# Optimization experiments

Measured on AMD Instinct MI355X. Metric: run time of the kernel, lower is better.

The kernel has to match this reference:

```python
import jax, jax.numpy as jnp
import numpy as np

NUM_HEADS = 8
NEG_INF = float(-2**32 + 1)  # matches torch padding value -2**32+1


def positional_encoding(B, T, d):
    # matches module: pe[:, :, 0::2] = sin(pos*div), pe[:, :, 1::2] = cos(pos*div)
    pos = jnp.arange(T, dtype=jnp.float32)[:, None]                      # (T, 1)
    div = jnp.exp(jnp.arange(0, d, 2, dtype=jnp.float32) * (-np.log(10000.0) / d))  # (d/2,)
    ang = pos * div                                                       # (T, d/2)
    pe = jnp.zeros((T, d), jnp.float32)
    pe = pe.at[:, 0::2].set(jnp.sin(ang)).at[:, 1::2].set(jnp.cos(ang))
    return jnp.broadcast_to(pe[None], (B, T, d))


def setup_inputs() -> dict:
    key = jax.random.key(0)
    ks = jax.random.split(key, 8)
    B, T, d, dff = 4, 2048, 128, 512
    s = 1.0 / np.sqrt(d)
    return {
        "x": jax.random.normal(ks[0], (B, T, d), jnp.float32),
        "W_Q": jax.random.normal(ks[1], (d, d), jnp.float32) * s,
        "W_K": jax.random.normal(ks[2], (d, d), jnp.float32) * s,
        "W_V": jax.random.normal(ks[3], (d, d), jnp.float32) * s,
        "W1": jax.random.normal(ks[4], (d, dff), jnp.float32) * s,
        "b1": jnp.zeros((dff,), jnp.float32),
        "W2": jax.random.normal(ks[5], (dff, d), jnp.float32) * (1.0 / np.sqrt(dff)),
        "b2": jnp.zeros((d,), jnp.float32),
    }


def reference(x, W_Q, W_K, W_V, W1, b1, W2, b2):
    B, T, d = x.shape
    H = NUM_HEADS
    e = d // H
    x = x + positional_encoding(B, T, d)           # residual later uses post-PE input
    Q = x @ W_Q
    K = x @ W_K
    V = x @ W_V
    # torch split(dim=2)+cat(dim=0) == (b t (h e)) -> (h b) t e; keep head axis separate
    Qh = Q.reshape(B, T, H, e).transpose(2, 0, 1, 3)   # (H, B, T, e)
    Kh = K.reshape(B, T, H, e).transpose(2, 0, 1, 3)
    Vh = V.reshape(B, T, H, e).transpose(2, 0, 1, 3)
    scores = jnp.einsum('hbqe,hbke->hbqk', Qh, Kh) / (T ** 0.5)  # scale by sqrt(time_step)
    mask = jnp.tril(jnp.ones((T, T), jnp.float32))
    scores = jnp.where(mask == 0, jnp.float32(NEG_INF), scores)
    # torch F.softmax(dim=1) on (H*B, T, T) -> softmax over QUERY axis (axis=2 here)
    attn = jax.nn.softmax(scores, axis=2)
    out = jnp.einsum('hbqk,hbke->hbqe', attn, Vh)      # (H, B, T, e)
    out = out.transpose(1, 2, 0, 3).reshape(B, T, d)   # cat heads back on feature dim
    ff = jnp.maximum(out @ W1 + b1, 0.0) @ W2 + b2
    return ff + x
```

## Files before the change

kernel.cpp:

```cpp
#include <hip/hip_runtime.h>
#include <math.h>
#include <stdint.h>

#define T_SEQ 2048
#define BATCH 4
#define DMODEL 128
#define DFF 512
#define NHEAD 8
#define EHEAD 16

#define QSCALE (0.022097086912079608f * 1.4426950408889634f)

typedef __attribute__((ext_vector_type(8))) short bf16x8;
typedef __attribute__((ext_vector_type(4))) short bf16x4;
typedef __attribute__((ext_vector_type(4))) float f32x4;

__device__ __forceinline__ short f2bf(float f) {
    uint32_t u = __float_as_uint(f);
    u = u + 0x7FFF + ((u >> 16) & 1);
    return (short)(u >> 16);
}
__device__ __forceinline__ short bftrunc(float f) {
    return (short)(__float_as_uint(f) >> 16);
}
__device__ __forceinline__ float bf2f(short s) {
    return __uint_as_float(((uint32_t)(unsigned short)s) << 16);
}
__device__ __forceinline__ float exp2_fast(float x) {
#if __has_builtin(__builtin_amdgcn_exp2f)
    return __builtin_amdgcn_exp2f(x);
#else
    float r; asm("v_exp_f32 %0, %1" : "=v"(r) : "v"(x)); return r;
#endif
}

#define MFMA16(A, B, C) __builtin_amdgcn_mfma_f32_16x16x32_bf16(A, B, C, 0, 0, 0)

__device__ __forceinline__ void gload16(const void* g, void* l) {
    __builtin_amdgcn_global_load_lds(
        (const __attribute__((address_space(1))) void*)g,
        (__attribute__((address_space(3))) void*)l, 16, 0, 0);
}

__device__ __forceinline__ int pair_rank(int id) {
    return (id < 256) ? id : 767 - id;
}

#define WP 136
__global__ __launch_bounds__(256) void k_qkv(const float* __restrict__ x,
                                             const float* __restrict__ WQ,
                                             const float* __restrict__ WK,
                                             const float* __restrict__ WV,
                                             const float* __restrict__ W1,
                                             const float* __restrict__ W2,
                                             float* __restrict__ xpe,
                                             short* __restrict__ Qh,
                                             short* __restrict__ Kh,
                                             short* __restrict__ Vs,
                                             short* __restrict__ W1t,
                                             short* __restrict__ W2t) {
    __shared__ __align__(16) short Wlds[128 * WP];
    int z = blockIdx.y;
    int tid = threadIdx.x;

    if (z == 3) {
        int base = (int)blockIdx.x * 256 + tid;
#pragma unroll
        for (int i = 0; i < 2; ++i) {
            int o = base + i * 32768;
            int n = o >> 7, k = o & 127;
            W1t[o] = f2bf(W1[k * 512 + n]);
        }
#pragma unroll
        for (int i = 0; i < 2; ++i) {
            int o = base + i * 32768;
            int n = o >> 9, k = o & 511;
            W2t[o] = f2bf(W2[k * 128 + n]);
        }
        return;
    }

    int wave = tid >> 6, lane = tid & 63;
    int g = lane >> 4, c = lane & 15;
    int row0 = blockIdx.x * 64 + wave * 16;
    int row = row0 + c;
    int tloc = row & (T_SEQ - 1);

    {
        const float* Wsrc = (z == 0) ? WQ : (z == 1) ? WK : WV;
        int k = tid & 127, n0 = (tid >> 7) * 64;
        const float* src = Wsrc + k * 128 + n0;
#pragma unroll
        for (int j = 0; j < 64; j += 4) {
            float4 wv = *(const float4*)(src + j);
            Wlds[(n0 + j + 0) * WP + k] = f2bf(wv.x);
            Wlds[(n0 + j + 1) * WP + k] = f2bf(wv.y);
            Wlds[(n0 + j + 2) * WP + k] = f2bf(wv.z);
            Wlds[(n0 + j + 3) * WP + k] = f2bf(wv.w);
        }
    }

    bf16x8 af[4];
#pragma unroll
    for (int kk = 0; kk < 4; ++kk) {
        int d0 = kk * 32 + 8 * g;
        const float* xb = x + (size_t)row * 128 + d0;
        float4 xa = *(const float4*)(xb);
        float4 xc = *(const float4*)(xb + 4);
        float vv[8] = {xa.x, xa.y, xa.z, xa.w, xc.x, xc.y, xc.z, xc.w};
#pragma unroll
        for (int p = 0; p < 4; ++p) {
            int d = d0 + 2 * p;
            float dv = __expf(-(float)d * (9.210340371976184f / 128.0f));
            float ang = (float)tloc * dv;
            vv[2 * p] += __sinf(ang);
            vv[2 * p + 1] += __cosf(ang);
        }
        if (z == 0) {
            float* xo = xpe + (size_t)row * 128 + d0;
            *(float4*)(xo) = make_float4(vv[0], vv[1], vv[2], vv[3]);
            *(float4*)(xo + 4) = make_float4(vv[4], vv[5], vv[6], vv[7]);
        }
#pragma unroll
        for (int j = 0; j < 8; ++j) af[kk][j] = f2bf(vv[j]);
    }
    __syncthreads();

    bf16x8 wf[8][4];
#pragma unroll
    for (int nt = 0; nt < 8; ++nt)
#pragma unroll
        for (int kk = 0; kk < 4; ++kk)
            wf[nt][kk] = *(const bf16x8*)(&Wlds[(nt * 16 + c) * WP + kk * 32 + 8 * g]);

    f32x4 acc[8];
#pragma unroll
    for (int nt = 0; nt < 8; ++nt) acc[nt] = (f32x4){0.f, 0.f, 0.f, 0.f};
#pragma unroll
    for (int kk = 0; kk < 4; ++kk)
#pragma unroll
        for (int nt = 0; nt < 8; ++nt)
            acc[nt] = MFMA16(af[kk], wf[nt][kk], acc[nt]);

    int b = row0 >> 11;
    int t0 = (row0 & (T_SEQ - 1)) + 4 * g;
    if (z < 2) {
        short* dst = (z == 0) ? Qh : Kh;
        float sc = (z == 0) ? QSCALE : 1.0f;
#pragma unroll
        for (int nt = 0; nt < 8; ++nt) {
            int hb = nt * 4 + b;
#pragma unroll
            for (int r = 0; r < 4; ++r)
                dst[(size_t)(hb * T_SEQ + t0 + r) * 16 + c] = f2bf(acc[nt][r] * sc);
        }
    } else {
#pragma unroll
        for (int nt = 0; nt < 8; ++nt) {
            int hb = nt * 4 + b;
            bf16x4 v;
#pragma unroll
            for (int r = 0; r < 4; ++r) v[r] = f2bf(acc[nt][r]);
            *(bf16x4*)(Vs + (size_t)(hb * 16 + c) * T_SEQ + t0) = v;
        }
    }
}
#undef WP

__global__ __launch_bounds__(512, 4) void k_csum(const short* __restrict__ Qh,
                                                 const short* __restrict__ Kh,
                                                 short* __restrict__ Vs) {
    __shared__ __align__(16) short Qt[2][4096];
    __shared__ float csLds[8][32];
    __shared__ float invl[128];
    const bf16x8 zz = {0, 0, 0, 0, 0, 0, 0, 0};
    const f32x4 z = {0.f, 0.f, 0.f, 0.f};

    int rank = pair_rank((int)blockIdx.x);
    int kc = rank >> 5, hb = rank & 31;
    int tid = threadIdx.x;
    int wave = tid >> 6, lane = tid & 63;
    int g = lane >> 4, c = lane & 15;
    int s = wave & 3, h = wave >> 2;
    int kw = kc * 128 + s * 32;
    const size_t hbT = (size_t)hb * T_SEQ;
    const short* Qg = Qh + hbT * 16;

    bf16x8 kfA = zz, kfB = zz;
    if (g < 2) {
        kfA = *(const bf16x8*)(Kh + (hbT + kw + c) * 16 + 8 * g);
        kfB = *(const bf16x8*)(Kh + (hbT + kw + 16 + c) * 16 + 8 * g);
    }

    int tstart = kc >> 1;
    gload16(Qg + (size_t)tstart * 4096 + tid * 8, &Qt[0][tid * 8]);
    __syncthreads();

    float csA = 0.f, csB = 0.f;
    for (int t = tstart; t < 8; ++t) {
        int buf = (t - tstart) & 1;
        if (t + 1 < 8)
            gload16(Qg + (size_t)(t + 1) * 4096 + tid * 8, &Qt[buf ^ 1][tid * 8]);
        const short* Qtb = &Qt[buf][0];
#pragma unroll
        for (int sj = 0; sj < 4; ++sj) {
            int ss = 4 * h + sj;
            int q32 = t * 256 + ss * 32;
            if (q32 + 31 < kw) continue;
            bf16x8 qfa = zz, qfb = zz;
            if (g < 2) {
                qfa = *(const bf16x8*)(Qtb + (ss * 32 + c) * 16 + g * 8);
                qfb = *(const bf16x8*)(Qtb + (ss * 32 + 16 + c) * 16 + g * 8);
            }
            f32x4 sA1 = MFMA16(qfa, kfA, z);
            f32x4 sB1 = MFMA16(qfa, kfB, z);
            f32x4 sA2 = MFMA16(qfb, kfA, z);
            f32x4 sB2 = MFMA16(qfb, kfB, z);
            if (q32 >= kw + 32) {
#pragma unroll
                for (int r = 0; r < 4; ++r) {
                    csA += exp2_fast(sA1[r]) + exp2_fast(sA2[r]);
                    csB += exp2_fast(sB1[r]) + exp2_fast(sB2[r]);
                }
            } else {
                int kA = kw + c, kB = kw + 16 + c;
#pragma unroll
                for (int r = 0; r < 4; ++r) {
                    int qa = q32 + 4 * g + r, qb = q32 + 16 + 4 * g + r;
                    csA += (qa >= kA) ? exp2_fast(sA1[r]) : 0.f;
                    csA += (qb >= kA) ? exp2_fast(sA2[r]) : 0.f;
                    csB += (qa >= kB) ? exp2_fast(sB1[r]) : 0.f;
                    csB += (qb >= kB) ? exp2_fast(sB2[r]) : 0.f;
                }
            }
        }
        __syncthreads();
    }

    csA += __shfl_xor(csA, 16);
    csA += __shfl_xor(csA, 32);
    csB += __shfl_xor(csB, 16);
    csB += __shfl_xor(csB, 32);
    if (lane < 32) csLds[wave][lane] = (lane < 16) ? csA : csB;
    __syncthreads();
    if (tid < 128) {
        int st = tid >> 5, col = tid & 31;
        invl[st * 32 + col] = 1.0f / (csLds[st][col] + csLds[st + 4][col]);
    }
    __syncthreads();
    if (tid < 256) {
        int e = tid >> 4, kcol = (tid & 15) * 8;
        size_t vo = (size_t)(hb * 16 + e) * T_SEQ + kc * 128 + kcol;
        bf16x8 v = *(bf16x8*)(Vs + vo);
        bf16x8 o;
#pragma unroll
        for (int j = 0; j < 8; ++j) o[j] = f2bf(bf2f(v[j]) * invl[kcol + j]);
        *(bf16x8*)(Vs + vo) = o;
    }
}

__global__ __launch_bounds__(512, 4) void k_attn(const short* __restrict__ Qh,
                                                 const short* __restrict__ Kh,
                                                 const short* __restrict__ Vs,
                                                 short* __restrict__ AObf) {
    __shared__ __align__(16) short Kt[2][4096];
    __shared__ __align__(16) short Vt[2][4096];
    const bf16x8 zz = {0, 0, 0, 0, 0, 0, 0, 0};
    const f32x4 z = {0.f, 0.f, 0.f, 0.f};

    int rank = pair_rank((int)blockIdx.x);
    int qn = 15 - (rank >> 5), hb = rank & 31;
    int h2 = hb >> 2, b = hb & 3;
    int tid = threadIdx.x;
    int wave = tid >> 6, lane = tid & 63;
    int g = lane >> 4, c = lane & 15;
    int s = wave & 3, h = wave >> 2;
    int q0w = qn * 128 + s * 32;
    const size_t hbT = (size_t)hb * T_SEQ;
    const short* Kg = Kh + hbT * 16;
    const short* Vg = Vs + (size_t)hb * 16 * T_SEQ;

    bf16x8 qf0 = zz, qf1 = zz;
    if (g < 2) {
        qf0 = *(const bf16x8*)(Qh + (hbT + q0w + c) * 16 + 8 * g);
        qf1 = *(const bf16x8*)(Qh + (hbT + q0w + 16 + c) * 16 + 8 * g);
    }

    int nT = (qn >> 1) + 1;

#define STAGE(bf, kt)                                                        \
    do {                                                                     \
        int k0s = (kt) * 256;                                                \
        gload16(Kg + (size_t)k0s * 16 + tid * 8, &Kt[bf][tid * 8]);          \
        int e0 = tid >> 5, jp = tid & 31, j0 = jp ^ (e0 & 7);                \
        gload16(Vg + (size_t)e0 * T_SEQ + k0s + j0 * 8, &Vt[bf][tid * 8]);   \
    } while (0)

    STAGE(0, 0);
    __syncthreads();

    f32x4 acc0 = z, acc1 = z;
    for (int t = 0; t < nT; ++t) {
        int buf = t & 1;
        if (t + 1 < nT) STAGE(buf ^ 1, t + 1);
        const short* Ktb = &Kt[buf][0];
        const short* Vtb = &Vt[buf][0];
#pragma unroll
        for (int sj = 0; sj < 4; ++sj) {
            int ss = 4 * h + sj;
            int k32 = t * 256 + ss * 32;
            if (k32 > q0w + 31) continue;
            bf16x8 kf0 = zz, kf1 = zz;
            if (g < 2) {
                kf0 = *(const bf16x8*)(Ktb + (ss * 32 + c) * 16 + g * 8);
                kf1 = *(const bf16x8*)(Ktb + (ss * 32 + 16 + c) * 16 + g * 8);
            }
            int ja = ss * 4 + (g >> 1);
            const short* vrow = Vtb + c * 256 + ((g & 1) << 2);
            bf16x4 v0 = *(const bf16x4*)(vrow + ((ja ^ (c & 7)) << 3));
            bf16x4 v1 = *(const bf16x4*)(vrow + (((ja + 2) ^ (c & 7)) << 3));
            f32x4 s0 = MFMA16(kf0, qf0, z);
            f32x4 s1 = MFMA16(kf1, qf0, z);
            f32x4 s2 = MFMA16(kf0, qf1, z);
            f32x4 s3 = MFMA16(kf1, qf1, z);
            bf16x8 aA, aB, vf;
            if (k32 + 31 <= q0w) {
#pragma unroll
                for (int r = 0; r < 4; ++r) {
                    aA[r] = bftrunc(exp2_fast(s0[r]));
                    aA[4 + r] = bftrunc(exp2_fast(s1[r]));
                    aB[r] = bftrunc(exp2_fast(s2[r]));
                    aB[4 + r] = bftrunc(exp2_fast(s3[r]));
                    vf[r] = v0[r];
                    vf[4 + r] = v1[r];
                }
            } else {
                int qa = q0w + c, qb = q0w + 16 + c;
                int ka = k32 + 4 * g, kb = k32 + 16 + 4 * g;
#pragma unroll
                for (int r = 0; r < 4; ++r) {
                    aA[r] = (ka + r <= qa) ? bftrunc(exp2_fast(s0[r])) : (short)0;
                    aA[4 + r] = (kb + r <= qa) ? bftrunc(exp2_fast(s1[r])) : (short)0;
                    aB[r] = (ka + r <= qb) ? bftrunc(exp2_fast(s2[r])) : (short)0;
                    aB[4 + r] = (kb + r <= qb) ? bftrunc(exp2_fast(s3[r])) : (short)0;
                    vf[r] = v0[r];
                    vf[4 + r] = v1[r];
                }
            }
            acc0 = MFMA16(aA, vf, acc0);
            acc1 = MFMA16(aB, vf, acc1);
        }
        __syncthreads();
    }
#undef STAGE

    float* Of = (float*)&Kt[0][0];
    if (h == 1) {
#pragma unroll
        for (int r = 0; r < 4; ++r) {
            Of[r * 256 + s * 64 + lane] = acc0[r];
            Of[(4 + r) * 256 + s * 64 + lane] = acc1[r];
        }
    }
    __syncthreads();
    if (h == 0) {
#pragma unroll
        for (int r = 0; r < 4; ++r) {
            acc0[r] += Of[r * 256 + s * 64 + lane];
            acc1[r] += Of[(4 + r) * 256 + s * 64 + lane];
        }
#pragma unroll
        for (int r = 0; r < 4; ++r) {
            AObf[(size_t)(b * T_SEQ + q0w + 4 * g + r) * DMODEL + h2 * EHEAD + c] = f2bf(acc0[r]);
            AObf[(size_t)(b * T_SEQ + q0w + 16 + 4 * g + r) * DMODEL + h2 * EHEAD + c] = f2bf(acc1[r]);
        }
    }
}

__global__ __launch_bounds__(256) void k_ff(const short* __restrict__ AObf,
                                            const short* __restrict__ W1t,
                                            const float* __restrict__ b1,
                                            const short* __restrict__ W2t,
                                            const float* __restrict__ b2,
                                            const float* __restrict__ xpe,
                                            float* __restrict__ out) {
    __shared__ __align__(16) short Fl[32][516];
    int w = threadIdx.x >> 6, lane = threadIdx.x & 63;
    int g = lane >> 4, c = lane & 15;
    int row0 = blockIdx.x * 32;

    {
        bf16x8 wf[8][4];
#pragma unroll
        for (int nt = 0; nt < 8; ++nt)
#pragma unroll
            for (int kk = 0; kk < 4; ++kk)
                wf[nt][kk] = *(const bf16x8*)(W1t + (w * 128 + nt * 16 + c) * 128 + kk * 32 + 8 * g);

#pragma unroll
        for (int ch = 0; ch < 2; ++ch) {
            int rbase = row0 + ch * 16;
            bf16x8 af[4];
#pragma unroll
            for (int kk = 0; kk < 4; ++kk)
                af[kk] = *(const bf16x8*)(AObf + (size_t)(rbase + c) * 128 + kk * 32 + 8 * g);

            f32x4 acc[8];
#pragma unroll
            for (int nt = 0; nt < 8; ++nt) acc[nt] = (f32x4){0.f, 0.f, 0.f, 0.f};
#pragma unroll
            for (int kk = 0; kk < 4; ++kk)
#pragma unroll
                for (int nt = 0; nt < 8; ++nt)
                    acc[nt] = MFMA16(af[kk], wf[nt][kk], acc[nt]);

#pragma unroll
            for (int nt = 0; nt < 8; ++nt) {
                int col = w * 128 + nt * 16 + c;
                float bb = b1[col];
#pragma unroll
                for (int r = 0; r < 4; ++r)
                    Fl[ch * 16 + 4 * g + r][col] = f2bf(fmaxf(acc[nt][r] + bb, 0.f));
            }
        }
    }
    __syncthreads();

    bf16x8 wf2[2][16];
#pragma unroll
    for (int nt = 0; nt < 2; ++nt)
#pragma unroll
        for (int kk = 0; kk < 16; ++kk)
            wf2[nt][kk] = *(const bf16x8*)(W2t + (w * 32 + nt * 16 + c) * 512 + kk * 32 + 8 * g);

#pragma unroll
    for (int ch = 0; ch < 2; ++ch) {
        int rbase = row0 + ch * 16;
        f32x4 acc2[2];
        acc2[0] = (f32x4){0.f, 0.f, 0.f, 0.f};
        acc2[1] = (f32x4){0.f, 0.f, 0.f, 0.f};
#pragma unroll
        for (int kk = 0; kk < 16; ++kk) {
            bf16x8 a = *(const bf16x8*)(&Fl[ch * 16 + c][kk * 32 + 8 * g]);
            acc2[0] = MFMA16(a, wf2[0][kk], acc2[0]);
            acc2[1] = MFMA16(a, wf2[1][kk], acc2[1]);
        }
#pragma unroll
        for (int nt = 0; nt < 2; ++nt) {
            int col = w * 32 + nt * 16 + c;
            float bb = b2[col];
#pragma unroll
            for (int r = 0; r < 4; ++r) {
                size_t o = (size_t)(rbase + 4 * g + r) * DMODEL + col;
                out[o] = acc2[nt][r] + bb + xpe[o];
            }
        }
    }
}

extern "C" void kernel_launch(void* const* d_in, const int* in_sizes, int n_in,
                              void* d_out, int out_size, void* d_ws, size_t ws_size,
                              hipStream_t stream) {
    const float* x  = (const float*)d_in[0];
    const float* WQ = (const float*)d_in[1];
    const float* WK = (const float*)d_in[2];
    const float* WV = (const float*)d_in[3];
    const float* W1 = (const float*)d_in[4];
    const float* b1 = (const float*)d_in[5];
    const float* W2 = (const float*)d_in[6];
    const float* b2 = (const float*)d_in[7];
    float* out = (float*)d_out;

    const size_t NTD = (size_t)BATCH * T_SEQ * DMODEL;
    float* xpe   = (float*)d_ws;
    short* Qh    = (short*)(xpe + NTD);
    short* Kh    = Qh + NTD;
    short* Vs    = Kh + NTD;
    short* AObf  = Vs + NTD;
    short* W1t   = AObf + NTD;
    short* W2t   = W1t + 65536;

    k_qkv<<<dim3(128, 4), dim3(256), 0, stream>>>(x, WQ, WK, WV, W1, W2,
                                                  xpe, Qh, Kh, Vs, W1t, W2t);

    k_csum<<<dim3(512), dim3(512), 0, stream>>>(Qh, Kh, Vs);

    k_attn<<<dim3(512), dim3(512), 0, stream>>>(Qh, Kh, Vs, AObf);

    k_ff<<<dim3(256), dim3(256), 0, stream>>>(AObf, W1t, b1, W2t, b2, xpe, out);
}
```

Baseline: 59.53 us.

## Halve attention and column-sum block tiles to 64 rows with 256-thread blocks

Splits the k_csum and k_attn work into 64-row tiles handled by 256-thread blocks, doubling the grid to 1024 blocks. A new quad_rank mapping orders blocks in serpentine groups of 256 so the triangular causal workload is balanced. Each thread now issues two staging loads per LDS tile to keep the same 256-row K/V/Q stages. This aims at better CU occupancy and finer load balancing, at the cost of each K/V tile being reloaded by twice as many blocks.

```diff
diff --git a/kernel.cpp b/kernel.cpp
--- a/kernel.cpp
+++ b/kernel.cpp
@@ -42,8 +42,9 @@
         (__attribute__((address_space(3))) void*)l, 16, 0, 0);
 }
 
-__device__ __forceinline__ int pair_rank(int id) {
-    return (id < 256) ? id : 767 - id;
+__device__ __forceinline__ int quad_rank(int id) {
+    int group = id >> 8, pos = id & 255;
+    return (group & 1) ? (((group + 1) << 8) - 1 - pos) : ((group << 8) + pos);
 }
 
 #define WP 136
@@ -167,22 +168,22 @@
 }
 #undef WP
 
-__global__ __launch_bounds__(512, 4) void k_csum(const short* __restrict__ Qh,
+__global__ __launch_bounds__(256, 4) void k_csum(const short* __restrict__ Qh,
                                                  const short* __restrict__ Kh,
                                                  short* __restrict__ Vs) {
     __shared__ __align__(16) short Qt[2][4096];
-    __shared__ float csLds[8][32];
-    __shared__ float invl[128];
+    __shared__ float csLds[4][32];
+    __shared__ float invl[64];
     const bf16x8 zz = {0, 0, 0, 0, 0, 0, 0, 0};
     const f32x4 z = {0.f, 0.f, 0.f, 0.f};
 
-    int rank = pair_rank((int)blockIdx.x);
+    int rank = quad_rank((int)blockIdx.x);
     int kc = rank >> 5, hb = rank & 31;
     int tid = threadIdx.x;
     int wave = tid >> 6, lane = tid & 63;
     int g = lane >> 4, c = lane & 15;
-    int s = wave & 3, h = wave >> 2;
-    int kw = kc * 128 + s * 32;
+    int s = wave & 1, h = wave >> 1;
+    int kw = kc * 64 + s * 32;
     const size_t hbT = (size_t)hb * T_SEQ;
     const short* Qg = Qh + hbT * 16;
 
@@ -192,15 +193,21 @@
         kfB = *(const bf16x8*)(Kh + (hbT + kw + 16 + c) * 16 + 8 * g);
     }
 
-    int tstart = kc >> 1;
-    gload16(Qg + (size_t)tstart * 4096 + tid * 8, &Qt[0][tid * 8]);
+#define QSTAGE(bf, tq)                                                       \
+    do {                                                                     \
+        const short* src = Qg + (size_t)(tq) * 4096;                         \
+        gload16(src + tid * 8, &Qt[bf][tid * 8]);                            \
+        gload16(src + 2048 + tid * 8, &Qt[bf][2048 + tid * 8]);              \
+    } while (0)
+
+    int tstart = kc >> 2;
+    QSTAGE(0, tstart);
     __syncthreads();
 
     float csA = 0.f, csB = 0.f;
     for (int t = tstart; t < 8; ++t) {
         int buf = (t - tstart) & 1;
-        if (t + 1 < 8)
-            gload16(Qg + (size_t)(t + 1) * 4096 + tid * 8, &Qt[buf ^ 1][tid * 8]);
+        if (t + 1 < 8) QSTAGE(buf ^ 1, t + 1);
         const short* Qtb = &Qt[buf][0];
 #pragma unroll
         for (int sj = 0; sj < 4; ++sj) {
@@ -236,6 +243,7 @@
         }
         __syncthreads();
     }
+#undef QSTAGE
 
     csA += __shfl_xor(csA, 16);
     csA += __shfl_xor(csA, 32);
@@ -243,14 +251,14 @@
     csB += __shfl_xor(csB, 32);
     if (lane < 32) csLds[wave][lane] = (lane < 16) ? csA : csB;
     __syncthreads();
+    if (tid < 64) {
+        int st = tid >> 5, col = tid & 31;
+        invl[tid] = 1.0f / (csLds[st][col] + csLds[st + 2][col]);
+    }
+    __syncthreads();
     if (tid < 128) {
-        int st = tid >> 5, col = tid & 31;
-        invl[st * 32 + col] = 1.0f / (csLds[st][col] + csLds[st + 4][col]);
-    }
-    __syncthreads();
-    if (tid < 256) {
-        int e = tid >> 4, kcol = (tid & 15) * 8;
-        size_t vo = (size_t)(hb * 16 + e) * T_SEQ + kc * 128 + kcol;
+        int e = tid >> 3, kcol = (tid & 7) * 8;
+        size_t vo = (size_t)(hb * 16 + e) * T_SEQ + kc * 64 + kcol;
         bf16x8 v = *(bf16x8*)(Vs + vo);
         bf16x8 o;
 #pragma unroll
@@ -259,7 +267,7 @@
     }
 }
 
-__global__ __launch_bounds__(512, 4) void k_attn(const short* __restrict__ Qh,
+__global__ __launch_bounds__(256, 4) void k_attn(const short* __restrict__ Qh,
                                                  const short* __restrict__ Kh,
                                                  const short* __restrict__ Vs,
                                                  short* __restrict__ AObf) {
@@ -268,14 +276,14 @@
     const bf16x8 zz = {0, 0, 0, 0, 0, 0, 0, 0};
     const f32x4 z = {0.f, 0.f, 0.f, 0.f};
 
-    int rank = pair_rank((int)blockIdx.x);
-    int qn = 15 - (rank >> 5), hb = rank & 31;
+    int rank = quad_rank((int)blockIdx.x);
+    int qn = 31 - (rank >> 5), hb = rank & 31;
     int h2 = hb >> 2, b = hb & 3;
     int tid = threadIdx.x;
     int wave = tid >> 6, lane = tid & 63;
     int g = lane >> 4, c = lane & 15;
-    int s = wave & 3, h = wave >> 2;
-    int q0w = qn * 128 + s * 32;
+    int s = wave & 1, h = wave >> 1;
+    int q0w = qn * 64 + s * 32;
     const size_t hbT = (size_t)hb * T_SEQ;
     const short* Kg = Kh + hbT * 16;
     const short* Vg = Vs + (size_t)hb * 16 * T_SEQ;
@@ -286,14 +294,20 @@
         qf1 = *(const bf16x8*)(Qh + (hbT + q0w + 16 + c) * 16 + 8 * g);
     }
 
-    int nT = (qn >> 1) + 1;
+    int nT = (qn >> 2) + 1;
 
 #define STAGE(bf, kt)                                                        \
     do {                                                                     \
         int k0s = (kt) * 256;                                                \
         gload16(Kg + (size_t)k0s * 16 + tid * 8, &Kt[bf][tid * 8]);          \
-        int e0 = tid >> 5, jp = tid & 31, j0 = jp ^ (e0 & 7);                \
+        gload16(Kg + (size_t)k0s * 16 + 2048 + tid * 8,                      \
+                &Kt[bf][2048 + tid * 8]);                                    \
+        int e0 = tid >> 5, j0 = (tid & 31) ^ (e0 & 7);                       \
         gload16(Vg + (size_t)e0 * T_SEQ + k0s + j0 * 8, &Vt[bf][tid * 8]);   \
+        int s1_ = tid + 256;                                                 \
+        int e1 = s1_ >> 5, j1 = (s1_ & 31) ^ (e1 & 7);                       \
+        gload16(Vg + (size_t)e1 * T_SEQ + k0s + j1 * 8,                      \
+                &Vt[bf][2048 + tid * 8]);                                    \
     } while (0)
 
     STAGE(0, 0);
@@ -358,16 +372,16 @@
     if (h == 1) {
 #pragma unroll
         for (int r = 0; r < 4; ++r) {
-            Of[r * 256 + s * 64 + lane] = acc0[r];
-            Of[(4 + r) * 256 + s * 64 + lane] = acc1[r];
+            Of[r * 128 + s * 64 + lane] = acc0[r];
+            Of[(4 + r) * 128 + s * 64 + lane] = acc1[r];
         }
     }
     __syncthreads();
     if (h == 0) {
 #pragma unroll
         for (int r = 0; r < 4; ++r) {
-            acc0[r] += Of[r * 256 + s * 64 + lane];
-            acc1[r] += Of[(4 + r) * 256 + s * 64 + lane];
+            acc0[r] += Of[r * 128 + s * 64 + lane];
+            acc1[r] += Of[(4 + r) * 128 + s * 64 + lane];
         }
 #pragma unroll
         for (int r = 0; r < 4; ++r) {
@@ -483,9 +497,9 @@
     k_qkv<<<dim3(128, 4), dim3(256), 0, stream>>>(x, WQ, WK, WV, W1, W2,
                                                   xpe, Qh, Kh, Vs, W1t, W2t);
 
-    k_csum<<<dim3(512), dim3(512), 0, stream>>>(Qh, Kh, Vs);
-
-    k_attn<<<dim3(512), dim3(512), 0, stream>>>(Qh, Kh, Vs, AObf);
+    k_csum<<<dim3(1024), dim3(256), 0, stream>>>(Qh, Kh, Vs);
+
+    k_attn<<<dim3(1024), dim3(256), 0, stream>>>(Qh, Kh, Vs, AObf);
 
     k_ff<<<dim3(256), dim3(256), 0, stream>>>(AObf, W1t, b1, W2t, b2, xpe, out);
 }
```

New measurement: 55.08 us (median of 2 runs). 1.08x faster.
